# Kernel optimization log

Hardware: AMD Instinct MI355X
Metric: run time of the kernel (lower is better)

The kernel has to match this reference:

```python
import jax, jax.numpy as jnp
import numpy as np

SHIFTS = [1, 3, 5, 7]
C = 16  # in_channels // 4
# -1 neighbor offsets for tmp1..tmp8 (dy, dx) in units of the dilation
OFFSETS = [(-1, -1), (-1, 0), (-1, 1), (0, 1), (1, 1), (1, 0), (1, -1), (0, -1)]


def setup_inputs() -> dict:
    key = jax.random.key(0)
    ks = jax.random.split(key, 32)
    d = {}
    d['cen'] = jax.random.normal(ks[0], (8, 64, 256, 256), jnp.float32)
    d['mas'] = jax.random.normal(ks[1], (8, 1, 256, 256), jnp.float32)
    d['in_conv_w'] = jax.random.normal(ks[2], (16, 64), jnp.float32) * 0.1
    d['in_conv_b'] = jax.random.normal(ks[3], (16,), jnp.float32) * 0.1
    for i, s in enumerate(SHIFTS):
        d[f'dw_w{s}'] = jax.random.normal(ks[4 + 2 * i], (16, 1, s, s), jnp.float32) * 0.1
        d[f'dw_b{s}'] = jax.random.normal(ks[5 + 2 * i], (16,), jnp.float32) * 0.1
    d['l1_w'] = jax.random.normal(ks[12], (4, 16, 4), jnp.float32) * 0.1
    d['l1_b'] = jax.random.normal(ks[13], (4, 16), jnp.float32) * 0.1
    d['l2_w'] = jax.random.normal(ks[14], (4, 16, 8), jnp.float32) * 0.1
    d['l2_b'] = jax.random.normal(ks[15], (4, 16), jnp.float32) * 0.1
    d['base_w'] = jax.random.normal(ks[16], (16, 4), jnp.float32) * 0.1
    d['bn_scale'] = jnp.ones((16,), jnp.float32)
    d['bn_bias'] = jnp.zeros((16,), jnp.float32)
    d['final_w'] = jax.random.normal(ks[17], (1, 16), jnp.float32) * 0.1
    d['final_b'] = jax.random.normal(ks[18], (1,), jnp.float32) * 0.1
    return d


def _dw_conv(x, w, b, pad):
    # depthwise conv, groups == channels
    y = jax.lax.conv_general_dilated(
        x, w, window_strides=(1, 1), padding=[(pad, pad), (pad, pad)],
        dimension_numbers=('NCHW', 'OIHW', 'NCHW'), feature_group_count=x.shape[1])
    return y + b[None, :, None, None]


def _shifted(x, dy, dx, d):
    # zero-padded shift: out(y,x) = in(y+dy, x+dx)
    H, W = x.shape[2], x.shape[3]
    p = jnp.pad(x, ((0, 0), (0, 0), (d, d), (d, d)))
    return p[:, :, d + dy:d + dy + H, d + dx:d + dx + W]


def _circ_shift(x, dw_w, dw_b, w1, b1, w2, b2, shift):
    x = _dw_conv(x, dw_w, dw_b, shift // 2)
    # tmp_k = x - x shifted by the k-th neighbor offset (dilation = shift)
    T = [x - _shifted(x, dy * shift, dx * shift, shift) for dy, dx in OFFSETS]
    # paired sums: S[k] = tmp_{k+1} + tmp_{k+5} (S repeats with period 4)
    S = [T[k] + T[k + 4] for k in range(4)]
    outs = []
    for k in range(8):  # fixed small structural loop
        feats = jnp.stack([S[(k + 1) % 4], S[(k + 3) % 4], S[(k + 2) % 4],
                           2.0 * T[(k + 4) % 8]], axis=2)  # (B,C,4,H,W)
        # grouped 1x1 conv (groups=C, 4C->C) == per-channel contraction over feature axis
        o = jnp.einsum('bcfhw,cf->bchw', feats, w1) + b1[None, :, None, None]
        outs.append(o * T[k])
    O = jnp.sort(jnp.stack(outs, axis=2), axis=2)  # (B,C,8,H,W) sorted over branch axis
    return jnp.einsum('bcfhw,cf->bchw', O, w2) + b2[None, :, None, None]


def reference(cen, mas, in_conv_w, in_conv_b, dw_w1, dw_b1, dw_w3, dw_b3,
              dw_w5, dw_b5, dw_w7, dw_b7, l1_w, l1_b, l2_w, l2_b,
              base_w, bn_scale, bn_bias, final_w, final_b):
    # in_conv: 1x1, in_channels -> C
    x = jnp.einsum('bihw,oi->bohw', cen, in_conv_w) + in_conv_b[None, :, None, None]
    dws = [(dw_w1, dw_b1), (dw_w3, dw_b3), (dw_w5, dw_b5), (dw_w7, dw_b7)]
    branches = [
        _circ_shift(x, dws[i][0], dws[i][1], l1_w[i], l1_b[i], l2_w[i], l2_b[i], SHIFTS[i])
        for i in range(len(SHIFTS))
    ]
    A = jnp.sort(jnp.stack(branches, axis=2), axis=2)  # (B,C,4,H,W)
    # out_conv: grouped 1x1 BaseConv (conv no-bias + BN(affine) + SiLU), then 1x1 -> 1, sigmoid
    y = jnp.einsum('bcfhw,cf->bchw', A, base_w)
    y = jax.nn.silu(y * bn_scale[None, :, None, None] + bn_bias[None, :, None, None])
    y = jnp.einsum('bchw,oc->bohw', y, final_w) + final_b[None, :, None, None]
    return jax.nn.sigmoid(y)
```

## Files before the change

### kernel.cpp

```cpp
#include <hip/hip_runtime.h>
#include <hip/hip_fp16.h>
#include <math.h>

#define HW 65536
#define PITCH 272
#define PLANE (PITCH * PITCH)

typedef float v2f __attribute__((ext_vector_type(2), aligned(8)));
typedef _Float16 h2 __attribute__((ext_vector_type(2)));

__device__ __forceinline__ h2 uh(unsigned u) { return __builtin_bit_cast(h2, u); }
__device__ __forceinline__ h2 lda(const ushort* p) { return *(const h2*)(const void*)p; }
__device__ __forceinline__ h2 ldu(const ushort* p) {
    unsigned lo = *(const unsigned*)(const void*)(p - 1);
    unsigned hi = *(const unsigned*)(const void*)(p + 1);
    unsigned r = (hi << 16) | (lo >> 16);
    return __builtin_bit_cast(h2, r);
}

#define CEH(a, b) { h2 _t = __builtin_elementwise_min(a, b); \
                    b = __builtin_elementwise_max(a, b); a = _t; }

__device__ __forceinline__ void sort8_h2(h2* v) {
    CEH(v[0], v[1]); CEH(v[2], v[3]); CEH(v[4], v[5]); CEH(v[6], v[7]);
    CEH(v[0], v[2]); CEH(v[1], v[3]); CEH(v[4], v[6]); CEH(v[5], v[7]);
    CEH(v[1], v[2]); CEH(v[5], v[6]); CEH(v[0], v[4]); CEH(v[3], v[7]);
    CEH(v[1], v[5]); CEH(v[2], v[6]);
    CEH(v[1], v[4]); CEH(v[3], v[6]);
    CEH(v[2], v[4]); CEH(v[3], v[5]);
    CEH(v[3], v[4]);
}
__device__ __forceinline__ void sort4_h2(h2* v) {
    CEH(v[0], v[1]); CEH(v[2], v[3]); CEH(v[0], v[2]); CEH(v[1], v[3]); CEH(v[1], v[2]);
}

__global__ __launch_bounds__(256) void k_pack(const float* __restrict__ l1w,
                                              const float* __restrict__ l1b,
                                              const float* __restrict__ l2w,
                                              const float* __restrict__ l2b,
                                              const float* __restrict__ bw,
                                              unsigned* __restrict__ wtab) {
    for (int t = threadIdx.x; t < 1088; t += 256) {
        float v = 0.f;
        if (t < 1024) {
            int c = t >> 6, i = (t >> 4) & 3, j = t & 15;
            if (j < 3)        v = l1w[i * 64 + c * 4 + j];
            else if (j == 3)  v = 2.f * l1w[i * 64 + c * 4 + 3];
            else if (j == 4)  v = l1b[i * 16 + c];
            else if (j < 13)  v = l2w[i * 128 + c * 8 + (j - 5)];
            else if (j == 13) v = l2b[i * 16 + c];
        } else {
            v = bw[t - 1024];
        }
        unsigned hs = (unsigned)__half_as_ushort(__float2half(v));
        wtab[t] = hs * 0x10001u;
    }
}

__global__ __launch_bounds__(256) void k_inconv(const float* __restrict__ cen,
                                                const float* __restrict__ w,
                                                const float* __restrict__ bias,
                                                __half* __restrict__ xh) {
    __shared__ float wl[1040];
    int tid = threadIdx.x;
    for (int t = tid; t < 1024; t += 256) wl[t] = w[(t & 15) * 64 + (t >> 4)];
    if (tid < 16) wl[1024 + tid] = bias[tid];
    __syncthreads();

    int pr = blockIdx.x * 256 + tid;
    int b_ = pr >> 15;
    int hw = (pr & 32767) * 2;
    const float* src = cen + (size_t)(b_ * 64) * HW + hw;

    v2f acc[16];
#pragma unroll
    for (int o = 0; o < 16; o++) { float bv = wl[1024 + o]; v2f t = {bv, bv}; acc[o] = t; }

#pragma unroll 4
    for (int i = 0; i < 64; i++) {
        v2f xv = *(const v2f*)(src + (size_t)i * HW);
        const float4* wq = (const float4*)&wl[i * 16];
#pragma unroll
        for (int g = 0; g < 4; g++) {
            float4 f = wq[g];
            acc[g * 4 + 0] += xv * f.x;
            acc[g * 4 + 1] += xv * f.y;
            acc[g * 4 + 2] += xv * f.z;
            acc[g * 4 + 3] += xv * f.w;
        }
    }
    __half* dst = xh + (size_t)(b_ * 16) * HW + hw;
#pragma unroll
    for (int o = 0; o < 16; o++)
        *(__half2*)(dst + (size_t)o * HW) = __floats2half2_rn(acc[o].x, acc[o].y);
}

__global__ __launch_bounds__(256) void k_dw(const __half* __restrict__ xh,
    const float* __restrict__ dw_w1, const float* __restrict__ dw_b1,
    const float* __restrict__ dw_w3, const float* __restrict__ dw_b3,
    const float* __restrict__ dw_w5, const float* __restrict__ dw_b5,
    const float* __restrict__ dw_w7, const float* __restrict__ dw_b7,
    __half* __restrict__ conv) {
    const int plane = blockIdx.y;
    const int c     = plane & 15;
    const int P0    = (blockIdx.x >> 2) * 68;
    const int Q0    = (blockIdx.x & 3) * 68;
    const int tid   = threadIdx.x;

    __shared__ float lx[74 * 76];
    const __half* xp = xh + (size_t)plane * HW;

    for (int t = tid; t < 74 * 74; t += 256) {
        int r = t / 74, cc = t - r * 74;
        int gy = P0 - 10 + r, gx = Q0 - 10 + cc;
        float v = 0.f;
        if ((unsigned)gy < 256u && (unsigned)gx < 256u) v = __half2float(xp[gy * 256 + gx]);
        lx[r * 76 + cc] = v;
    }
    __syncthreads();

    const float* W7 = dw_w7 + c * 49;
    const float* W5 = dw_w5 + c * 25;
    const float* W3 = dw_w3 + c * 9;
    const float  W1 = dw_w1[c];
    const float  B1 = dw_b1[c], B3 = dw_b3[c], B5 = dw_b5[c], B7 = dw_b7[c];

    for (int u = tid; u < 68 * 34; u += 256) {
        int row = u / 34;
        int pc0 = (u - row * 34) * 2;
        v2f c7v = {0, 0}, c5v = {0, 0}, c3v = {0, 0}, c1v = {0, 0};
#pragma unroll
        for (int a = 0; a < 7; a++) {
            const float* rp = &lx[(row + a) * 76 + pc0];
            v2f q0 = *(const v2f*)rp;
            v2f q1 = *(const v2f*)(rp + 2);
            v2f q2 = *(const v2f*)(rp + 4);
            v2f q3 = *(const v2f*)(rp + 6);
            float v8 = rp[8];
            float v[9] = {q0.x, q0.y, q1.x, q1.y, q2.x, q2.y, q3.x, q3.y, v8};
#pragma unroll
            for (int bb = 0; bb < 7; bb++) {
                v2f vv = {v[bb], v[bb + 1]};
                c7v += vv * W7[a * 7 + bb];
            }
            if (a >= 1 && a <= 5) {
#pragma unroll
                for (int bb = 0; bb < 5; bb++) {
                    v2f vv = {v[bb + 1], v[bb + 2]};
                    c5v += vv * W5[(a - 1) * 5 + bb];
                }
            }
            if (a >= 2 && a <= 4) {
#pragma unroll
                for (int bb = 0; bb < 3; bb++) {
                    v2f vv = {v[bb + 2], v[bb + 3]};
                    c3v += vv * W3[(a - 2) * 3 + bb];
                }
            }
            if (a == 3) {
                v2f vv = {v[3], v[4]};
                c1v = vv * W1;
            }
        }
        int py = P0 + row, px = Q0 + pc0;
        int iy = py - 7, ix = px - 7;
        bool rin = (unsigned)iy < 256u;
        bool in0 = rin && (unsigned)ix < 256u;
        bool in1 = rin && (unsigned)(ix + 1) < 256u;
        size_t o = (size_t)(plane * 4) * PLANE + (size_t)py * PITCH + px;
        *(__half2*)&conv[o]              = __floats2half2_rn(in0 ? c1v.x + B1 : 0.f, in1 ? c1v.y + B1 : 0.f);
        *(__half2*)&conv[o + PLANE]      = __floats2half2_rn(in0 ? c3v.x + B3 : 0.f, in1 ? c3v.y + B3 : 0.f);
        *(__half2*)&conv[o + 2 * PLANE]  = __floats2half2_rn(in0 ? c5v.x + B5 : 0.f, in1 ? c5v.y + B5 : 0.f);
        *(__half2*)&conv[o + 3 * PLANE]  = __floats2half2_rn(in0 ? c7v.x + B7 : 0.f, in1 ? c7v.y + B7 : 0.f);
    }
}

__global__ __launch_bounds__(256) void k_mach(const __half* __restrict__ conv,
                                              const unsigned* __restrict__ wtab,
                                              const float* __restrict__ bns,
                                              const float* __restrict__ bnb,
                                              const float* __restrict__ fw,
                                              const float* __restrict__ fb,
                                              float* __restrict__ out) {
    const int b_ = blockIdx.y;
    const int pr = blockIdx.x * 256 + threadIdx.x;
    const int gy = pr >> 7, gx = (pr & 127) * 2;
    const int e0 = (gy + 7) * PITCH + (gx + 7);
    const ushort* cb = (const ushort*)conv + (size_t)(b_ * 64) * PLANE + e0;

    float fyx = fb[0], fyy = fb[0];

    for (int c = 0; c < 16; c++) {
        const ushort* cvp = cb + (size_t)(c * 4) * PLANE;
        h2 bh[4];
#pragma unroll
        for (int i = 0; i < 4; i++) {
            const int s = 1 + 2 * i;
            const ushort* pb = cvp + (size_t)i * PLANE;
            h2 ctr = ldu(pb);
            h2 n0 = lda(pb - s * PITCH - s);
            h2 n1 = ldu(pb - s * PITCH);
            h2 n2 = lda(pb - s * PITCH + s);
            h2 n3 = lda(pb + s);
            h2 n4 = lda(pb + s * PITCH + s);
            h2 n5 = ldu(pb + s * PITCH);
            h2 n6 = lda(pb + s * PITCH - s);
            h2 n7 = lda(pb - s);

            h2 T[8];
            T[0] = ctr - n0; T[1] = ctr - n1; T[2] = ctr - n2; T[3] = ctr - n3;
            T[4] = ctr - n4; T[5] = ctr - n5; T[6] = ctr - n6; T[7] = ctr - n7;
            h2 S[4];
#pragma unroll
            for (int k = 0; k < 4; k++) S[k] = T[k] + T[k + 4];

            const unsigned* wt = wtab + ((c << 2) + i) * 16;
            h2 w10 = uh(wt[0]), w11 = uh(wt[1]), w12 = uh(wt[2]);
            h2 w13x2 = uh(wt[3]), bb1 = uh(wt[4]);

            h2 R[4];
#pragma unroll
            for (int m = 0; m < 4; m++) {
                h2 r = S[(m + 2) & 3] * w12 + bb1;
                r = S[(m + 3) & 3] * w11 + r;
                r = S[(m + 1) & 3] * w10 + r;
                R[m] = r;
            }
            h2 h8[8];
#pragma unroll
            for (int k = 0; k < 8; k++)
                h8[k] = (T[(k + 4) & 7] * w13x2 + R[k & 3]) * T[k];
            sort8_h2(h8);

            h2 acc = uh(wt[13]);
#pragma unroll
            for (int k = 0; k < 8; k++) acc += h8[k] * uh(wt[5 + k]);
            bh[i] = acc;
        }
        sort4_h2(bh);
        h2 yv = bh[0] * uh(wtab[1024 + (c << 2)]);
#pragma unroll
        for (int k = 1; k < 4; k++) yv = bh[k] * uh(wtab[1024 + (c << 2) + k]) + yv;

        float zx = fmaf((float)yv.x, bns[c], bnb[c]);
        float zy = fmaf((float)yv.y, bns[c], bnb[c]);
        float sx = zx / (1.f + __expf(-zx));
        float sy = zy / (1.f + __expf(-zy));
        fyx = fmaf(sx, fw[c], fyx);
        fyy = fmaf(sy, fw[c], fyy);
    }
    float2 r;
    r.x = 1.f / (1.f + __expf(-fyx));
    r.y = 1.f / (1.f + __expf(-fyy));
    *(float2*)&out[((long)b_ << 16) + pr * 2] = r;
}

extern "C" void kernel_launch(void* const* d_in, const int* in_sizes, int n_in,
                              void* d_out, int out_size, void* d_ws, size_t ws_size,
                              hipStream_t stream) {
    (void)in_sizes; (void)n_in; (void)out_size; (void)ws_size;
    const float* cen   = (const float*)d_in[0];
    const float* in_w  = (const float*)d_in[2];
    const float* in_b  = (const float*)d_in[3];
    const float* dw_w1 = (const float*)d_in[4];
    const float* dw_b1 = (const float*)d_in[5];
    const float* dw_w3 = (const float*)d_in[6];
    const float* dw_b3 = (const float*)d_in[7];
    const float* dw_w5 = (const float*)d_in[8];
    const float* dw_b5 = (const float*)d_in[9];
    const float* dw_w7 = (const float*)d_in[10];
    const float* dw_b7 = (const float*)d_in[11];
    const float* l1w   = (const float*)d_in[12];
    const float* l1b   = (const float*)d_in[13];
    const float* l2w   = (const float*)d_in[14];
    const float* l2b   = (const float*)d_in[15];
    const float* bw    = (const float*)d_in[16];
    const float* bns   = (const float*)d_in[17];
    const float* bnb   = (const float*)d_in[18];
    const float* fw    = (const float*)d_in[19];
    const float* fb    = (const float*)d_in[20];

    __half*   xh   = (__half*)d_ws;
    __half*   conv = (__half*)((char*)d_ws + (size_t)16777216);
    unsigned* wtab = (unsigned*)((char*)d_ws + (size_t)16777216 + (size_t)75759616);
    float*    out  = (float*)d_out;

    k_pack<<<1, 256, 0, stream>>>(l1w, l1b, l2w, l2b, bw, wtab);
    k_inconv<<<1024, 256, 0, stream>>>(cen, in_w, in_b, xh);
    k_dw<<<dim3(16, 128), 256, 0, stream>>>(xh, dw_w1, dw_b1, dw_w3, dw_b3,
                                            dw_w5, dw_b5, dw_w7, dw_b7, conv);
    k_mach<<<dim3(128, 8), 256, 0, stream>>>(conv, wtab, bns, bnb, fw, fb, out);
}
```

Before: 348.4 us.

## Stage conv tiles in LDS for k_mach, shrink dw tiles, widen inconv loads

After: 368.3 us. +5.7%, slower.

```diff
diff --git a/kernel.cpp b/kernel.cpp
--- a/kernel.cpp
+++ b/kernel.cpp
@@ -10,13 +10,6 @@
 typedef _Float16 h2 __attribute__((ext_vector_type(2)));
 
 __device__ __forceinline__ h2 uh(unsigned u) { return __builtin_bit_cast(h2, u); }
-__device__ __forceinline__ h2 lda(const ushort* p) { return *(const h2*)(const void*)p; }
-__device__ __forceinline__ h2 ldu(const ushort* p) {
-    unsigned lo = *(const unsigned*)(const void*)(p - 1);
-    unsigned hi = *(const unsigned*)(const void*)(p + 1);
-    unsigned r = (hi << 16) | (lo >> 16);
-    return __builtin_bit_cast(h2, r);
-}
 
 #define CEH(a, b) { h2 _t = __builtin_elementwise_min(a, b); \
                     b = __builtin_elementwise_max(a, b); a = _t; }
@@ -57,42 +50,50 @@
     }
 }
 
-__global__ __launch_bounds__(256) void k_inconv(const float* __restrict__ cen,
-                                                const float* __restrict__ w,
-                                                const float* __restrict__ bias,
-                                                __half* __restrict__ xh) {
+__global__ __launch_bounds__(256, 4) void k_inconv(const float* __restrict__ cen,
+                                                   const float* __restrict__ w,
+                                                   const float* __restrict__ bias,
+                                                   __half* __restrict__ xh) {
     __shared__ float wl[1040];
     int tid = threadIdx.x;
     for (int t = tid; t < 1024; t += 256) wl[t] = w[(t & 15) * 64 + (t >> 4)];
     if (tid < 16) wl[1024 + tid] = bias[tid];
     __syncthreads();
 
-    int pr = blockIdx.x * 256 + tid;
-    int b_ = pr >> 15;
-    int hw = (pr & 32767) * 2;
+    int q  = blockIdx.x * 256 + tid;
+    int b_ = q >> 14;
+    int hw = (q & 16383) * 4;
     const float* src = cen + (size_t)(b_ * 64) * HW + hw;
 
-    v2f acc[16];
-#pragma unroll
-    for (int o = 0; o < 16; o++) { float bv = wl[1024 + o]; v2f t = {bv, bv}; acc[o] = t; }
+    float4 acc[16];
+#pragma unroll
+    for (int o = 0; o < 16; o++) { float bv = wl[1024 + o]; acc[o] = make_float4(bv, bv, bv, bv); }
 
 #pragma unroll 4
     for (int i = 0; i < 64; i++) {
-        v2f xv = *(const v2f*)(src + (size_t)i * HW);
+        float4 xv = *(const float4*)(src + (size_t)i * HW);
         const float4* wq = (const float4*)&wl[i * 16];
 #pragma unroll
         for (int g = 0; g < 4; g++) {
             float4 f = wq[g];
-            acc[g * 4 + 0] += xv * f.x;
-            acc[g * 4 + 1] += xv * f.y;
-            acc[g * 4 + 2] += xv * f.z;
-            acc[g * 4 + 3] += xv * f.w;
+            acc[g * 4 + 0].x += xv.x * f.x; acc[g * 4 + 0].y += xv.y * f.x;
+            acc[g * 4 + 0].z += xv.z * f.x; acc[g * 4 + 0].w += xv.w * f.x;
+            acc[g * 4 + 1].x += xv.x * f.y; acc[g * 4 + 1].y += xv.y * f.y;
+            acc[g * 4 + 1].z += xv.z * f.y; acc[g * 4 + 1].w += xv.w * f.y;
+            acc[g * 4 + 2].x += xv.x * f.z; acc[g * 4 + 2].y += xv.y * f.z;
+            acc[g * 4 + 2].z += xv.z * f.z; acc[g * 4 + 2].w += xv.w * f.z;
+            acc[g * 4 + 3].x += xv.x * f.w; acc[g * 4 + 3].y += xv.y * f.w;
+            acc[g * 4 + 3].z += xv.z * f.w; acc[g * 4 + 3].w += xv.w * f.w;
         }
     }
     __half* dst = xh + (size_t)(b_ * 16) * HW + hw;
 #pragma unroll
-    for (int o = 0; o < 16; o++)
-        *(__half2*)(dst + (size_t)o * HW) = __floats2half2_rn(acc[o].x, acc[o].y);
+    for (int o = 0; o < 16; o++) {
+        uint2 pk;
+        pk.x = __builtin_bit_cast(unsigned, __floats2half2_rn(acc[o].x, acc[o].y));
+        pk.y = __builtin_bit_cast(unsigned, __floats2half2_rn(acc[o].z, acc[o].w));
+        *(uint2*)(dst + (size_t)o * HW) = pk;
+    }
 }
 
 __global__ __launch_bounds__(256) void k_dw(const __half* __restrict__ xh,
@@ -103,19 +104,21 @@
     __half* __restrict__ conv) {
     const int plane = blockIdx.y;
     const int c     = plane & 15;
-    const int P0    = (blockIdx.x >> 2) * 68;
-    const int Q0    = (blockIdx.x & 3) * 68;
+    const int P0    = (blockIdx.x >> 3) * 34;
+    const int Q0    = (blockIdx.x & 7) * 34;
     const int tid   = threadIdx.x;
 
-    __shared__ float lx[74 * 76];
+    __shared__ float lx[40 * 44];
     const __half* xp = xh + (size_t)plane * HW;
 
-    for (int t = tid; t < 74 * 74; t += 256) {
-        int r = t / 74, cc = t - r * 74;
-        int gy = P0 - 10 + r, gx = Q0 - 10 + cc;
-        float v = 0.f;
-        if ((unsigned)gy < 256u && (unsigned)gx < 256u) v = __half2float(xp[gy * 256 + gx]);
-        lx[r * 76 + cc] = v;
+    for (int t = tid; t < 40 * 21; t += 256) {
+        int r = t / 21, d = t - r * 21;
+        int gy = P0 - 10 + r, gx = Q0 - 10 + 2 * d;
+        float2 v = make_float2(0.f, 0.f);
+        if ((unsigned)gy < 256u && (unsigned)gx < 256u)
+            v = __half22float2(*(const __half2*)(xp + gy * 256 + gx));
+        lx[r * 44 + 2 * d]     = v.x;
+        lx[r * 44 + 2 * d + 1] = v.y;
     }
     __syncthreads();
 
@@ -125,13 +128,13 @@
     const float  W1 = dw_w1[c];
     const float  B1 = dw_b1[c], B3 = dw_b3[c], B5 = dw_b5[c], B7 = dw_b7[c];
 
-    for (int u = tid; u < 68 * 34; u += 256) {
-        int row = u / 34;
-        int pc0 = (u - row * 34) * 2;
+    for (int u = tid; u < 34 * 17; u += 256) {
+        int row = u / 17;
+        int pc0 = (u - row * 17) * 2;
         v2f c7v = {0, 0}, c5v = {0, 0}, c3v = {0, 0}, c1v = {0, 0};
 #pragma unroll
         for (int a = 0; a < 7; a++) {
-            const float* rp = &lx[(row + a) * 76 + pc0];
+            const float* rp = &lx[(row + a) * 44 + pc0];
             v2f q0 = *(const v2f*)rp;
             v2f q1 = *(const v2f*)(rp + 2);
             v2f q2 = *(const v2f*)(rp + 4);
@@ -168,44 +171,77 @@
         bool in0 = rin && (unsigned)ix < 256u;
         bool in1 = rin && (unsigned)(ix + 1) < 256u;
         size_t o = (size_t)(plane * 4) * PLANE + (size_t)py * PITCH + px;
-        *(__half2*)&conv[o]              = __floats2half2_rn(in0 ? c1v.x + B1 : 0.f, in1 ? c1v.y + B1 : 0.f);
-        *(__half2*)&conv[o + PLANE]      = __floats2half2_rn(in0 ? c3v.x + B3 : 0.f, in1 ? c3v.y + B3 : 0.f);
-        *(__half2*)&conv[o + 2 * PLANE]  = __floats2half2_rn(in0 ? c5v.x + B5 : 0.f, in1 ? c5v.y + B5 : 0.f);
-        *(__half2*)&conv[o + 3 * PLANE]  = __floats2half2_rn(in0 ? c7v.x + B7 : 0.f, in1 ? c7v.y + B7 : 0.f);
-    }
-}
-
-__global__ __launch_bounds__(256) void k_mach(const __half* __restrict__ conv,
-                                              const unsigned* __restrict__ wtab,
-                                              const float* __restrict__ bns,
-                                              const float* __restrict__ bnb,
-                                              const float* __restrict__ fw,
-                                              const float* __restrict__ fb,
-                                              float* __restrict__ out) {
-    const int b_ = blockIdx.y;
-    const int pr = blockIdx.x * 256 + threadIdx.x;
-    const int gy = pr >> 7, gx = (pr & 127) * 2;
-    const int e0 = (gy + 7) * PITCH + (gx + 7);
-    const ushort* cb = (const ushort*)conv + (size_t)(b_ * 64) * PLANE + e0;
+        *(__half2*)&conv[o]             = __floats2half2_rn(in0 ? c1v.x + B1 : 0.f, in1 ? c1v.y + B1 : 0.f);
+        *(__half2*)&conv[o + PLANE]     = __floats2half2_rn(in0 ? c3v.x + B3 : 0.f, in1 ? c3v.y + B3 : 0.f);
+        *(__half2*)&conv[o + 2 * PLANE] = __floats2half2_rn(in0 ? c5v.x + B5 : 0.f, in1 ? c5v.y + B5 : 0.f);
+        *(__half2*)&conv[o + 3 * PLANE] = __floats2half2_rn(in0 ? c7v.x + B7 : 0.f, in1 ? c7v.y + B7 : 0.f);
+    }
+}
+
+__global__ __launch_bounds__(512, 4) void k_mach(const __half* __restrict__ conv,
+                                                 const unsigned* __restrict__ wtab,
+                                                 const float* __restrict__ bns,
+                                                 const float* __restrict__ bnb,
+                                                 const float* __restrict__ fw,
+                                                 const float* __restrict__ fb,
+                                                 float* __restrict__ out) {
+    const int b_  = blockIdx.y;
+    const int ty0 = (blockIdx.x >> 3) * 32;
+    const int tx0 = (blockIdx.x & 7) * 32;
+    const int tid = threadIdx.x;
+    const int py  = tid >> 4;
+    const int pxp = tid & 15;
+
+    __shared__ __align__(16) unsigned convt[4 * 46 * 24];
 
     float fyx = fb[0], fyy = fb[0];
 
     for (int c = 0; c < 16; c++) {
-        const ushort* cvp = cb + (size_t)(c * 4) * PLANE;
+        if (c) __syncthreads();
+        {
+            const size_t pb4 = (size_t)(b_ * 64 + c * 4) * PLANE;
+#pragma unroll
+            for (int j = 0; j < 5; j++) {
+                int t = tid + j * 512;
+                if (t < 2208) {
+                    int i  = t / 552;
+                    int rm = t - i * 552;
+                    int r  = rm / 12;
+                    int d2 = rm - r * 12;
+                    size_t E = pb4 + (size_t)i * PLANE + (size_t)(ty0 + r) * PITCH + tx0 + 4 * d2;
+                    ((uint2*)convt)[t] = *(const uint2*)(conv + E);
+                }
+            }
+        }
+        __syncthreads();
+
         h2 bh[4];
 #pragma unroll
         for (int i = 0; i < 4; i++) {
             const int s = 1 + 2 * i;
-            const ushort* pb = cvp + (size_t)i * PLANE;
-            h2 ctr = ldu(pb);
-            h2 n0 = lda(pb - s * PITCH - s);
-            h2 n1 = ldu(pb - s * PITCH);
-            h2 n2 = lda(pb - s * PITCH + s);
-            h2 n3 = lda(pb + s);
-            h2 n4 = lda(pb + s * PITCH + s);
-            h2 n5 = ldu(pb + s * PITCH);
-            h2 n6 = lda(pb + s * PITCH - s);
-            h2 n7 = lda(pb - s);
+            const unsigned* pl = convt + i * 1104;
+            const int q    = pxp + (7 - s) / 2;
+            const int topb = (py + 7 - s) * 24 + q;
+            const int midb = (py + 7) * 24 + q;
+            const int botb = (py + 7 + s) * 24 + q;
+
+            unsigned tt[8], tm[8], tb[8];
+#pragma unroll
+            for (int k = 0; k <= s; k++) {
+                tt[k] = pl[topb + k];
+                tm[k] = pl[midb + k];
+                tb[k] = pl[botb + k];
+            }
+            const int m = s >> 1;
+            h2 n0  = uh(tt[0]);
+            h2 n1  = uh((tt[m] >> 16) | (tt[m + 1] << 16));
+            h2 n2  = uh(tt[s]);
+            h2 n7  = uh(tm[0]);
+            h2 ctr = uh((tm[m] >> 16) | (tm[m + 1] << 16));
+            h2 n3  = uh(tm[s]);
+            h2 n6  = uh(tb[0]);
+            h2 n5  = uh((tb[m] >> 16) | (tb[m + 1] << 16));
+            h2 n4  = uh(tb[s]);
 
             h2 T[8];
             T[0] = ctr - n0; T[1] = ctr - n1; T[2] = ctr - n2; T[3] = ctr - n3;
@@ -220,11 +256,11 @@
 
             h2 R[4];
 #pragma unroll
-            for (int m = 0; m < 4; m++) {
-                h2 r = S[(m + 2) & 3] * w12 + bb1;
-                r = S[(m + 3) & 3] * w11 + r;
-                r = S[(m + 1) & 3] * w10 + r;
-                R[m] = r;
+            for (int mm = 0; mm < 4; mm++) {
+                h2 r = S[(mm + 2) & 3] * w12 + bb1;
+                r = S[(mm + 3) & 3] * w11 + r;
+                r = S[(mm + 1) & 3] * w10 + r;
+                R[mm] = r;
             }
             h2 h8[8];
 #pragma unroll
@@ -252,7 +288,7 @@
     float2 r;
     r.x = 1.f / (1.f + __expf(-fyx));
     r.y = 1.f / (1.f + __expf(-fyy));
-    *(float2*)&out[((long)b_ << 16) + pr * 2] = r;
+    *(float2*)&out[((long)b_ << 16) + (ty0 + py) * 256 + tx0 + 2 * pxp] = r;
 }
 
 extern "C" void kernel_launch(void* const* d_in, const int* in_sizes, int n_in,
@@ -286,8 +322,8 @@
     float*    out  = (float*)d_out;
 
     k_pack<<<1, 256, 0, stream>>>(l1w, l1b, l2w, l2b, bw, wtab);
-    k_inconv<<<1024, 256, 0, stream>>>(cen, in_w, in_b, xh);
-    k_dw<<<dim3(16, 128), 256, 0, stream>>>(xh, dw_w1, dw_b1, dw_w3, dw_b3,
+    k_inconv<<<512, 256, 0, stream>>>(cen, in_w, in_b, xh);
+    k_dw<<<dim3(64, 128), 256, 0, stream>>>(xh, dw_w1, dw_b1, dw_w3, dw_b3,
                                             dw_w5, dw_b5, dw_w7, dw_b7, conv);
-    k_mach<<<dim3(128, 8), 256, 0, stream>>>(conv, wtab, bns, bnb, fw, fb, out);
-}
+    k_mach<<<dim3(64, 8), 512, 0, stream>>>(conv, wtab, bns, bnb, fw, fb, out);
+}
```
